# Performance work log

Measured on AMD Instinct MI355X. Metric: run time of the kernel, lower is better.

The kernel has to match this reference:

```python
import jax, jax.numpy as jnp
import numpy as np

N_NODES = 256
BATCH = 8
N_IN = 64
N_HID = 128
N_OUT = 64


def _incidence():
    # fully connected graph without self-loops (standard NRI setup)
    off_diag = np.ones((N_NODES, N_NODES)) - np.eye(N_NODES)
    recv_idx, send_idx = np.where(off_diag)  # each [E], E = N*(N-1)
    eye = np.eye(N_NODES, dtype=np.float32)
    rel_rec = eye[recv_idx]   # [E, N] one-hot
    rel_send = eye[send_idx]  # [E, N] one-hot
    return jnp.asarray(rel_rec), jnp.asarray(rel_send)


def setup_inputs() -> dict:
    key = jax.random.key(0)
    k_x, k_w1, k_w2 = jax.random.split(key, 3)
    rel_rec, rel_send = _incidence()
    x = jax.random.normal(k_x, (BATCH, N_NODES, N_IN), dtype=jnp.float32)
    # torch.nn.Linear weights: [out_features, in_features]
    W1 = jax.random.normal(k_w1, (N_HID, 2 * N_IN), dtype=jnp.float32) / np.sqrt(2 * N_IN)
    b1 = jnp.zeros((N_HID,), dtype=jnp.float32)
    W2 = jax.random.normal(k_w2, (N_OUT, N_HID), dtype=jnp.float32) / np.sqrt(N_HID)
    b2 = jnp.zeros((N_OUT,), dtype=jnp.float32)
    return {"x": x, "rel_rec": rel_rec, "rel_send": rel_send,
            "W1": W1, "b1": b1, "W2": W2, "b2": b2}


def reference(x, rel_rec, rel_send, W1, b1, W2, b2):
    # node2edge: dense one-hot matmuls (gather of node features per edge)
    receivers = jnp.einsum('en,bnf->bef', rel_rec, x)   # [B, E, n_in]
    senders = jnp.einsum('en,bnf->bef', rel_send, x)    # [B, E, n_in]
    edges = jnp.concatenate([senders, receivers], axis=-1)  # [B, E, 2*n_in]
    # 2-layer MLP: Linear -> ReLU -> Linear (torch Linear: y = x @ W.T + b)
    h = jax.nn.relu(jnp.einsum('bef,hf->beh', edges, W1) + b1)
    out = jnp.einsum('beh,oh->beo', h, W2) + b2          # [B, E, n_out]
    return out
```

## Files before the change

kernel.cpp:

```cpp
#include <hip/hip_runtime.h>
#include <hip/hip_bf16.h>


using frag_t  = __attribute__((ext_vector_type(8))) short;
using f32x4   = __attribute__((ext_vector_type(4))) float;
using f32x16  = __attribute__((ext_vector_type(16))) float;
using ushort8 = __attribute__((ext_vector_type(8))) unsigned short;

__device__ inline unsigned short f2bf(float f) {
    union { __hip_bfloat16 h; unsigned short u; } v;
    v.h = __float2bfloat16(f);
    return v.u;
}

__device__ inline ushort8 pack8(f32x4 a, f32x4 b) {
    ushort8 o;
    o[0] = f2bf(a[0]); o[1] = f2bf(a[1]); o[2] = f2bf(a[2]); o[3] = f2bf(a[3]);
    o[4] = f2bf(b[0]); o[5] = f2bf(b[1]); o[6] = f2bf(b[2]); o[7] = f2bf(b[3]);
    return o;
}

__device__ inline frag_t packfrag(f32x4 a, f32x4 b) {
    union { ushort8 u; frag_t f; } v; v.u = pack8(a, b); return v.f;
}

__device__ inline int swz(int row, int c) { return c ^ (row & 7); }

__global__ __launch_bounds__(256)
void nri_mlp_fused(const float* __restrict__ x,
                   const float* __restrict__ W1,
                   const float* __restrict__ b1,
                   const float* __restrict__ W2,
                   const float* __restrict__ b2,
                   float* __restrict__ out) {
    __shared__ unsigned short W1s[128 * 128];
    __shared__ unsigned short W2s[64 * 128];

    const int tid  = threadIdx.x;
    const int wave = tid >> 6;
    const int lane = tid & 63;
    const int hi   = lane >> 5;
    const int l5   = lane & 31;

    const int bx = blockIdx.x;
    const int b  = bx / 255;
    const int eb = (bx - b * 255) * 256;
    const int e0 = eb + wave * 64;

    const float* xb = x + b * (256 * 64);

    #pragma unroll
    for (int i = 0; i < 8; ++i) {
        int cid  = tid + i * 256;
        int row  = cid >> 4;
        int c    = cid & 15;
        const float* s = W1 + row * 128 + c * 8;
        *(ushort8*)&W1s[row * 128 + swz(row, c) * 8] =
            pack8(*(const f32x4*)s, *(const f32x4*)(s + 4));
    }
    #pragma unroll
    for (int i = 0; i < 4; ++i) {
        int cid  = tid + i * 256;
        int row  = cid >> 4;
        int c    = cid & 15;
        int base = 32 * (c >> 2) + 16 * ((c >> 1) & 1) + 4 * (c & 1);
        const float* s = W2 + row * 128 + base;
        *(ushort8*)&W2s[row * 128 + swz(row, c) * 8] =
            pack8(*(const f32x4*)s, *(const f32x4*)(s + 8));
    }
    __syncthreads();

    #pragma unroll 1
    for (int g = 0; g < 2; ++g) {
        int e    = e0 + g * 32 + l5;
        int recv = e / 255;
        int kk   = e - recv * 255;
        int send = kk + (kk >= recv ? 1 : 0);

        frag_t af[8];
        #pragma unroll
        for (int ks = 0; ks < 8; ++ks) {
            int node = (ks < 4) ? send : recv;
            const float* s = xb + node * 64 + (ks & 3) * 16 + hi * 8;
            af[ks] = packfrag(*(const f32x4*)s, *(const f32x4*)(s + 4));
        }

        f32x16 acc[4];
        #pragma unroll
        for (int cb = 0; cb < 4; ++cb)
            #pragma unroll
            for (int r = 0; r < 16; ++r) acc[cb][r] = 0.f;
        #pragma unroll
        for (int ks = 0; ks < 8; ++ks) {
            int chunk = 2 * ks + hi;
            #pragma unroll
            for (int cb = 0; cb < 4; ++cb) {
                int row = 32 * cb + l5;
                frag_t w1 = *(const frag_t*)&W1s[row * 128 + swz(row, chunk) * 8];
                acc[cb] = __builtin_amdgcn_mfma_f32_32x32x16_bf16(w1, af[ks], acc[cb], 0, 0, 0);
            }
        }

        const float* b1p = b1;
        asm volatile("" : "+s"(b1p));
        frag_t hf[8];
        #pragma unroll
        for (int cb = 0; cb < 4; ++cb) {
            f32x4 t[4];
            #pragma unroll
            for (int m = 0; m < 4; ++m) {
                f32x4 bv = *(const f32x4*)(b1p + 32 * cb + 8 * m + 4 * hi);
                #pragma unroll
                for (int q = 0; q < 4; ++q) {
                    float v = acc[cb][4 * m + q] + bv[q];
                    t[m][q] = v > 0.f ? v : 0.f;
                }
            }
            hf[2 * cb]     = packfrag(t[0], t[1]);
            hf[2 * cb + 1] = packfrag(t[2], t[3]);
        }

        f32x16 acc2[2];
        #pragma unroll
        for (int c2 = 0; c2 < 2; ++c2)
            #pragma unroll
            for (int r = 0; r < 16; ++r) acc2[c2][r] = 0.f;
        #pragma unroll
        for (int ks = 0; ks < 8; ++ks) {
            int chunk = 2 * ks + hi;
            #pragma unroll
            for (int c2 = 0; c2 < 2; ++c2) {
                int row = 32 * c2 + l5;
                frag_t w2 = *(const frag_t*)&W2s[row * 128 + swz(row, chunk) * 8];
                acc2[c2] = __builtin_amdgcn_mfma_f32_32x32x16_bf16(w2, hf[ks], acc2[c2], 0, 0, 0);
            }
        }

        const float* b2p = b2;
        asm volatile("" : "+s"(b2p));
        float* ob = out + ((long)b * 65280 + e) * 64;
        #pragma unroll
        for (int c2 = 0; c2 < 2; ++c2) {
            #pragma unroll
            for (int m = 0; m < 4; ++m) {
                f32x4 bv = *(const f32x4*)(b2p + 32 * c2 + 8 * m + 4 * hi);
                f32x4 v;
                #pragma unroll
                for (int q = 0; q < 4; ++q) v[q] = acc2[c2][4 * m + q] + bv[q];
                *(f32x4*)&ob[32 * c2 + 8 * m + 4 * hi] = v;
            }
        }
    }
}

extern "C" void kernel_launch(void* const* d_in, const int* in_sizes, int n_in,
                              void* d_out, int out_size, void* d_ws, size_t ws_size,
                              hipStream_t stream) {
    const float* x  = (const float*)d_in[0];
    const float* W1 = (const float*)d_in[3];
    const float* b1 = (const float*)d_in[4];
    const float* W2 = (const float*)d_in[5];
    const float* b2 = (const float*)d_in[6];
    (void)d_ws; (void)ws_size; (void)in_sizes; (void)n_in; (void)out_size;
    float* out = (float*)d_out;

    nri_mlp_fused<<<2040, 256, 0, stream>>>(x, W1, b1, W2, b2, out);
}
```

Before: 259.7 us.

## Stage node features in LDS, enlarge blocks, transpose second MFMA for coalesced stores

```diff
diff --git a/kernel.cpp b/kernel.cpp
--- a/kernel.cpp
+++ b/kernel.cpp
@@ -24,17 +24,17 @@
     union { ushort8 u; frag_t f; } v; v.u = pack8(a, b); return v.f;
 }
 
-__device__ inline int swz(int row, int c) { return c ^ (row & 7); }
-
-__global__ __launch_bounds__(256)
+__global__ __launch_bounds__(384)
 void nri_mlp_fused(const float* __restrict__ x,
                    const float* __restrict__ W1,
                    const float* __restrict__ b1,
                    const float* __restrict__ W2,
                    const float* __restrict__ b2,
                    float* __restrict__ out) {
-    __shared__ unsigned short W1s[128 * 128];
-    __shared__ unsigned short W2s[64 * 128];
+    extern __shared__ unsigned short smem[];
+    unsigned short* W1s = smem;
+    unsigned short* W2s = smem + 128 * 128;
+    unsigned short* Xs  = smem + 128 * 128 + 64 * 128;
 
     const int tid  = threadIdx.x;
     const int wave = tid >> 6;
@@ -43,32 +43,46 @@
     const int l5   = lane & 31;
 
     const int bx = blockIdx.x;
-    const int b  = bx / 255;
-    const int eb = (bx - b * 255) * 256;
+    const int b  = bx / 170;
+    const int eb = (bx - b * 170) * 384;
     const int e0 = eb + wave * 64;
 
     const float* xb = x + b * (256 * 64);
 
     #pragma unroll
-    for (int i = 0; i < 8; ++i) {
-        int cid  = tid + i * 256;
-        int row  = cid >> 4;
-        int c    = cid & 15;
-        const float* s = W1 + row * 128 + c * 8;
-        *(ushort8*)&W1s[row * 128 + swz(row, c) * 8] =
-            pack8(*(const f32x4*)s, *(const f32x4*)(s + 4));
+    for (int i = 0; i < 6; ++i) {
+        int cid = tid + i * 384;
+        if (cid < 2048) {
+            int row = cid >> 4, c = cid & 15;
+            const float* s = W1 + row * 128 + c * 8;
+            *(ushort8*)&W1s[row * 128 + (c ^ (row & 7)) * 8] =
+                pack8(*(const f32x4*)s, *(const f32x4*)(s + 4));
+        }
     }
     #pragma unroll
-    for (int i = 0; i < 4; ++i) {
-        int cid  = tid + i * 256;
-        int row  = cid >> 4;
-        int c    = cid & 15;
-        int base = 32 * (c >> 2) + 16 * ((c >> 1) & 1) + 4 * (c & 1);
-        const float* s = W2 + row * 128 + base;
-        *(ushort8*)&W2s[row * 128 + swz(row, c) * 8] =
-            pack8(*(const f32x4*)s, *(const f32x4*)(s + 8));
+    for (int i = 0; i < 3; ++i) {
+        int cid = tid + i * 384;
+        if (cid < 1024) {
+            int row = cid >> 4, c = cid & 15;
+            int base = 32 * (c >> 2) + 16 * ((c >> 1) & 1) + 4 * (c & 1);
+            const float* s = W2 + row * 128 + base;
+            *(ushort8*)&W2s[row * 128 + (c ^ (row & 7)) * 8] =
+                pack8(*(const f32x4*)s, *(const f32x4*)(s + 8));
+        }
+    }
+    #pragma unroll
+    for (int i = 0; i < 6; ++i) {
+        int cid = tid + i * 384;
+        if (cid < 2048) {
+            int node = cid >> 3, c = cid & 7;
+            const float* s = xb + node * 64 + c * 8;
+            *(ushort8*)&Xs[node * 64 + (c ^ (node & 7)) * 8] =
+                pack8(*(const f32x4*)s, *(const f32x4*)(s + 4));
+        }
     }
     __syncthreads();
+
+    float b2v[2] = { b2[l5], b2[32 + l5] };
 
     #pragma unroll 1
     for (int g = 0; g < 2; ++g) {
@@ -81,8 +95,8 @@
         #pragma unroll
         for (int ks = 0; ks < 8; ++ks) {
             int node = (ks < 4) ? send : recv;
-            const float* s = xb + node * 64 + (ks & 3) * 16 + hi * 8;
-            af[ks] = packfrag(*(const f32x4*)s, *(const f32x4*)(s + 4));
+            int c    = (ks & 3) * 2 + hi;
+            af[ks] = *(const frag_t*)&Xs[node * 64 + (c ^ (node & 7)) * 8];
         }
 
         f32x16 acc[4];
@@ -96,7 +110,7 @@
             #pragma unroll
             for (int cb = 0; cb < 4; ++cb) {
                 int row = 32 * cb + l5;
-                frag_t w1 = *(const frag_t*)&W1s[row * 128 + swz(row, chunk) * 8];
+                frag_t w1 = *(const frag_t*)&W1s[row * 128 + (chunk ^ (row & 7)) * 8];
                 acc[cb] = __builtin_amdgcn_mfma_f32_32x32x16_bf16(w1, af[ks], acc[cb], 0, 0, 0);
             }
         }
@@ -131,23 +145,18 @@
             #pragma unroll
             for (int c2 = 0; c2 < 2; ++c2) {
                 int row = 32 * c2 + l5;
-                frag_t w2 = *(const frag_t*)&W2s[row * 128 + swz(row, chunk) * 8];
-                acc2[c2] = __builtin_amdgcn_mfma_f32_32x32x16_bf16(w2, hf[ks], acc2[c2], 0, 0, 0);
+                frag_t w2 = *(const frag_t*)&W2s[row * 128 + (chunk ^ (row & 7)) * 8];
+                acc2[c2] = __builtin_amdgcn_mfma_f32_32x32x16_bf16(hf[ks], w2, acc2[c2], 0, 0, 0);
             }
         }
 
-        const float* b2p = b2;
-        asm volatile("" : "+s"(b2p));
-        float* ob = out + ((long)b * 65280 + e) * 64;
+        float* ob = out + ((long)b * 65280 + e0 + g * 32) * 64;
         #pragma unroll
         for (int c2 = 0; c2 < 2; ++c2) {
             #pragma unroll
-            for (int m = 0; m < 4; ++m) {
-                f32x4 bv = *(const f32x4*)(b2p + 32 * c2 + 8 * m + 4 * hi);
-                f32x4 v;
-                #pragma unroll
-                for (int q = 0; q < 4; ++q) v[q] = acc2[c2][4 * m + q] + bv[q];
-                *(f32x4*)&ob[32 * c2 + 8 * m + 4 * hi] = v;
+            for (int r = 0; r < 16; ++r) {
+                int eo = (r & 3) + 8 * (r >> 2) + 4 * hi;
+                ob[eo * 64 + 32 * c2 + l5] = acc2[c2][r] + b2v[c2];
             }
         }
     }
@@ -164,5 +173,11 @@
     (void)d_ws; (void)ws_size; (void)in_sizes; (void)n_in; (void)out_size;
     float* out = (float*)d_out;
 
-    nri_mlp_fused<<<2040, 256, 0, stream>>>(x, W1, b1, W2, b2, out);
+    static bool attr_set = false;
+    if (!attr_set) {
+        hipFuncSetAttribute(reinterpret_cast<const void*>(nri_mlp_fused),
+                            hipFuncAttributeMaxDynamicSharedMemorySize, 81920);
+        attr_set = true;
+    }
+    nri_mlp_fused<<<1360, 384, 81920, stream>>>(x, W1, b1, W2, b2, out);
 }
```

New measurement: 238.1 us. 8.3% less time.
